# Performance work log

Measured on AMD Instinct MI355X. Metric: run time of the kernel, lower is better.

Reference implementation:

```python
import jax, jax.numpy as jnp
import numpy as np

N, E, H, HEADS, HD, L = 4096, 65536, 128, 4, 32, 4
NF, GF, EF, B = 16, 8, 4, 1


def _ln(x, g, b, eps=1e-5):
    mu = x.mean(-1, keepdims=True)
    v = ((x - mu) ** 2).mean(-1, keepdims=True)
    return (x - mu) * jax.lax.rsqrt(v + eps) * g + b


def _lin(x, W, b=None):
    y = x @ W.T
    return y if b is None else y + b


def _gelu(x):
    return jax.nn.gelu(x, approximate=False)


def setup_inputs() -> dict:
    key = jax.random.key(0)
    ks = iter(jax.random.split(key, 64))
    def rn(shape, s=0.05):
        return jax.random.normal(next(ks), shape, jnp.float32) * s
    inp = {}
    inp['x'] = jax.random.normal(next(ks), (N, NF), jnp.float32)
    inp['edge_index'] = jax.random.randint(next(ks), (2, E), 0, N, dtype=jnp.int32)
    inp['edge_attr'] = jax.random.normal(next(ks), (E, EF), jnp.float32)
    inp['u'] = jax.random.normal(next(ks), (1, GF), jnp.float32)
    inp['acting_mask'] = jax.random.randint(next(ks), (N,), 0, 2, dtype=jnp.int32).astype(bool)
    inp['h_tiles'] = jnp.zeros((N, H), jnp.float32)
    inp['batch'] = jnp.zeros((N,), jnp.int32)
    inp['turn_frac'] = jax.random.uniform(next(ks), (1,), jnp.float32)
    # node / global encoders
    inp['ne_W'] = rn((H, NF + 1)); inp['ne_b'] = jnp.zeros((H,)); inp['ne_g'] = jnp.ones((H,)); inp['ne_be'] = jnp.zeros((H,))
    inp['ge_W'] = rn((H, GF)); inp['ge_b'] = jnp.zeros((H,)); inp['ge_g'] = jnp.ones((H,)); inp['ge_be'] = jnp.zeros((H,))
    # GRUCell
    inp['gru_Wih'] = rn((3 * H, H)); inp['gru_bih'] = jnp.zeros((3 * H,))
    inp['gru_Whh'] = rn((3 * H, H)); inp['gru_bhh'] = jnp.zeros((3 * H,))
    # stacked GATv2 layers
    inp['gat_Wl'] = rn((L, H, H)); inp['gat_bl'] = jnp.zeros((L, H))
    inp['gat_Wr'] = rn((L, H, H)); inp['gat_br'] = jnp.zeros((L, H))
    inp['gat_We'] = rn((L, H, EF))
    inp['gat_att'] = rn((L, HEADS, HD))
    inp['gat_bias'] = jnp.zeros((L, H))
    inp['ln_g'] = jnp.ones((L, H)); inp['ln_b'] = jnp.zeros((L, H))
    # global MHA
    inp['attn_Win'] = rn((3 * H, H)); inp['attn_bin'] = jnp.zeros((3 * H,))
    inp['attn_Wout'] = rn((H, H)); inp['attn_bout'] = jnp.zeros((H,))
    inp['lng_g'] = jnp.ones((H,)); inp['lng_b'] = jnp.zeros((H,))
    # heads (edge_in = 2H + EF)
    inp['mv_W1'] = rn((H, 2 * H + EF)); inp['mv_b1'] = jnp.zeros((H,))
    inp['mv_W2'] = rn((1, H)); inp['mv_b2'] = jnp.zeros((1,))
    inp['fr_W1'] = rn((H, 2 * H + EF)); inp['fr_b1'] = jnp.zeros((H,))
    inp['fr_W2'] = rn((2, H)); inp['fr_b2'] = jnp.zeros((2,))
    inp['vl_W1'] = rn((H, 2 * H)); inp['vl_b1'] = jnp.zeros((H,))
    inp['vl_W2'] = rn((1, H)); inp['vl_b2'] = jnp.zeros((1,))
    return inp


def reference(x, edge_index, edge_attr, u, acting_mask, h_tiles, batch, turn_frac,
              ne_W, ne_b, ne_g, ne_be, ge_W, ge_b, ge_g, ge_be,
              gru_Wih, gru_bih, gru_Whh, gru_bhh,
              gat_Wl, gat_bl, gat_Wr, gat_br, gat_We, gat_att, gat_bias, ln_g, ln_b,
              attn_Win, attn_bin, attn_Wout, attn_bout, lng_g, lng_b,
              mv_W1, mv_b1, mv_W2, mv_b2, fr_W1, fr_b1, fr_W2, fr_b2,
              vl_W1, vl_b1, vl_W2, vl_b2):
    Nn = x.shape[0]
    src, dst = edge_index[0], edge_index[1]
    xa = jnp.concatenate([x, jnp.broadcast_to(turn_frac, (Nn, 1))], -1)
    h = _gelu(_ln(_lin(xa, ne_W, ne_b), ne_g, ne_be))
    ue = _gelu(_ln(_lin(u, ge_W, ge_b), ge_g, ge_be))
    h = h + ue[batch]
    # GRUCell (torch semantics)
    gi = _lin(h, gru_Wih, gru_bih)
    gh = _lin(h_tiles, gru_Whh, gru_bhh)
    i_r, i_z, i_n = jnp.split(gi, 3, -1)
    h_r, h_z, h_n = jnp.split(gh, 3, -1)
    r = jax.nn.sigmoid(i_r + h_r)
    z = jax.nn.sigmoid(i_z + h_z)
    n = jnp.tanh(i_n + r * h_n)
    h = (1.0 - z) * n + z * h_tiles
    h_tiles_new = jax.lax.stop_gradient(h)
    # stacked GATv2 message passing (eval mode: no dropout)
    for l in range(L):
        xl = _lin(h, gat_Wl[l], gat_bl[l]).reshape(Nn, HEADS, HD)   # source messages
        xr = _lin(h, gat_Wr[l], gat_br[l]).reshape(Nn, HEADS, HD)   # target
        ee = (edge_attr @ gat_We[l].T).reshape(-1, HEADS, HD)
        m = xl[src]                                                 # [E,heads,hd]
        s = jax.nn.leaky_relu(m + xr[dst] + ee, negative_slope=0.2)
        score = (s * gat_att[l]).sum(-1)                            # [E,heads]
        mx = jax.ops.segment_max(score, dst, num_segments=Nn)
        mx = jnp.where(jnp.isfinite(mx), mx, 0.0)
        ex = jnp.exp(score - mx[dst])
        den = jax.ops.segment_sum(ex, dst, num_segments=Nn)
        alpha_e = ex / (den[dst] + 1e-16)
        agg = jax.ops.segment_sum(alpha_e[..., None] * m, dst, num_segments=Nn)
        h_mp = agg.reshape(Nn, H) + gat_bias[l]
        h = _ln(h + h_mp, ln_g[l], ln_b[l])
    # global self-attention over all nodes as one sequence
    q, k, v = jnp.split(_lin(h, attn_Win, attn_bin), 3, -1)
    q = q.reshape(Nn, HEADS, HD); k = k.reshape(Nn, HEADS, HD); v = v.reshape(Nn, HEADS, HD)
    att = jax.nn.softmax(jnp.einsum('nhd,mhd->hnm', q, k) / np.float32(np.sqrt(HD)), axis=-1)
    ao = jnp.einsum('hnm,mhd->nhd', att, v).reshape(Nn, H)
    h = _ln(h + _lin(ao, attn_Wout, attn_bout), lng_g, lng_b)
    # edge heads
    eemb = jnp.concatenate([h[src], h[dst], edge_attr], -1)         # [E, 2H+EF]
    move_logits = _lin(_gelu(_lin(eemb, mv_W1, mv_b1)), mv_W2, mv_b2)[:, 0]
    fp = _lin(_gelu(_lin(eemb, fr_W1, fr_b1)), fr_W2, fr_b2)
    alpha = jax.nn.softplus(fp[:, 0]) + 1e-4
    beta = jax.nn.softplus(fp[:, 1]) + 1e-4
    # value head (global mean pool + masked acting pool)
    cnt = jax.ops.segment_sum(jnp.ones((Nn, 1), h.dtype), batch, num_segments=B)
    gpool = jax.ops.segment_sum(h, batch, num_segments=B) / cnt
    ah = jnp.where(acting_mask[:, None], h, 0.0)
    asum = jax.ops.segment_sum(ah, batch, num_segments=B) / cnt
    acnt = jnp.maximum(jax.ops.segment_sum(acting_mask[:, None].astype(h.dtype), batch, num_segments=B) / cnt, 1e-6)
    apool = asum / acnt
    vin = jnp.concatenate([gpool, apool], -1)
    value = _lin(_gelu(_lin(vin, vl_W1, vl_b1)), vl_W2, vl_b2)[:, 0]
    return move_logits, alpha, beta, value, h_tiles_new
```

## Files before the change

### kernel.cpp

```cpp
#include <hip/hip_runtime.h>
#include <math.h>


#define NN 4096
#define EE 65536
#define HH 128
#define NHEADS 4
#define HDIM 32
#define NLAYERS 4
#define NFEAT 16
#define GFEAT 8
#define EFEAT 4
#define KS 4
#define KPAD 296
#define XSTR 136
#define KSTR 40
#define VSTR 72

typedef short bf16x8 __attribute__((ext_vector_type(8)));
typedef float f32x4  __attribute__((ext_vector_type(4)));
union UB { uint4 u; bf16x8 v; };

__device__ __forceinline__ float gelu_f(float x){
  return 0.5f * x * (1.0f + erff(x * 0.7071067811865475f));
}
__device__ __forceinline__ float gelu_fast(float x){
  float u = x + 0.044715f * x * x * x;
  float t = __expf(-1.5957691216f * u);
  return x / (1.0f + t);
}
__device__ __forceinline__ float sigm_fast(float x){ return 1.0f / (1.0f + __expf(-x)); }
__device__ __forceinline__ float tanh_fast(float x){
  float t = __expf(-2.0f * fmaxf(x, -40.0f));
  return 1.0f - 2.0f * t / (1.0f + t);
}
__device__ __forceinline__ float softplus_f(float x){ return x > 20.0f ? x : log1pf(expf(x)); }
__device__ __forceinline__ unsigned short f2bf(float x){
  unsigned u = __float_as_uint(x);
  unsigned r = (u + 0x7FFFu + ((u >> 16) & 1u)) >> 16;
  return (unsigned short)r;
}
__device__ __forceinline__ float bf2f(unsigned short x){
  return __uint_as_float(((unsigned)x) << 16);
}
__device__ __forceinline__ unsigned pack2bf(float lo, float hi){
  unsigned a = (__float_as_uint(lo) + 0x8000u) >> 16;
  unsigned b = (__float_as_uint(hi) + 0x8000u) & 0xFFFF0000u;
  return a | b;
}

__device__ __forceinline__ float block_sum128(float v, float* red){
  int j = threadIdx.x;
  red[j] = v; __syncthreads();
  for (int s = 64; s > 0; s >>= 1){
    if (j < s) red[j] += red[j + s];
    __syncthreads();
  }
  float r = red[0];
  __syncthreads();
  return r;
}

__global__ void k_hist(const int* __restrict__ ei, int* __restrict__ cnt){
  int e = blockIdx.x * 256 + threadIdx.x;
  if (e < EE) atomicAdd(&cnt[ei[EE + e]], 1);
}

__global__ void k_scan(const int* __restrict__ cnt, int* __restrict__ off, int* __restrict__ cur){
  __shared__ int part[256];
  int t = threadIdx.x;
  int local[16];
  int s = 0;
  #pragma unroll
  for (int i = 0; i < 16; i++){ local[i] = s; s += cnt[t * 16 + i]; }
  part[t] = s; __syncthreads();
  for (int o = 1; o < 256; o <<= 1){
    int v = (t >= o) ? part[t - o] : 0;
    __syncthreads();
    part[t] += v;
    __syncthreads();
  }
  int base = part[t] - s;
  #pragma unroll
  for (int i = 0; i < 16; i++){ int o = base + local[i]; off[t * 16 + i] = o; cur[t * 16 + i] = o; }
  if (t == 255) off[NN] = part[255];
}

__global__ void k_scatter(const int* __restrict__ ei, int* __restrict__ cur,
                          int* __restrict__ srcs, int* __restrict__ rank){
  int e = blockIdx.x * 256 + threadIdx.x;
  if (e < EE){
    int d = ei[EE + e];
    int p = atomicAdd(&cur[d], 1);
    srcs[p] = ei[e];
    rank[e] = p;
  }
}

__global__ void k_wprep(const float* __restrict__ Wih, const float* __restrict__ Whh,
                        const float* __restrict__ Wl, const float* __restrict__ Wr,
                        const float* __restrict__ Win, const float* __restrict__ Wout,
                        const float* __restrict__ tiles,
                        const float* __restrict__ bl, const float* __restrict__ br,
                        const float* __restrict__ ea,
                        const float* __restrict__ mvW1, const float* __restrict__ frW1,
                        unsigned short* __restrict__ wbuf, unsigned short* __restrict__ tilesb,
                        float* __restrict__ blrc,
                        unsigned short* __restrict__ wbE, unsigned short* __restrict__ eab,
                        int* __restrict__ cnt, float* __restrict__ gsum){
  int i = blockIdx.x * 256 + threadIdx.x;
  if (i < 49152){ wbuf[i] = f2bf(Wih[i]); }
  else if (i < 98304){ int j = i - 49152; wbuf[49152 + j] = f2bf(Whh[j]); }
  else if (i < 229376){
    int j = i - 98304;
    int l = j >> 15, rem = j & 32767, m = rem >> 7, k = rem & 127;
    float v = (m < 128) ? Wl[l * 16384 + m * 128 + k] : Wr[l * 16384 + (m - 128) * 128 + k];
    wbuf[98304 + j] = f2bf(v);
  }
  else if (i < 278528){ int j = i - 229376; wbuf[229376 + j] = f2bf(Win[j]); }
  else if (i < 294912){ int j = i - 278528; wbuf[278528 + j] = f2bf(Wout[j]); }
  else if (i < 819200){ int j = i - 294912; tilesb[j] = f2bf(tiles[j]); }
  else if (i < 820224){
    int j = i - 819200;
    int l = j >> 8, m = j & 255;
    blrc[j] = (m < 128) ? bl[l * 128 + m] : br[l * 128 + m - 128];
  }
  else if (i < 896000){
    int j = i - 820224;
    int n = j / KPAD, k = j - n * KPAD;
    float v = 0.0f;
    if (k < 2 * HH + EFEAT) v = (n < HH) ? mvW1[n * (2 * HH + EFEAT) + k]
                                         : frW1[(n - HH) * (2 * HH + EFEAT) + k];
    wbE[j] = f2bf(v);
  }
  else if (i < 1158144){
    int j = i - 896000;
    eab[j] = f2bf(ea[j]);
  }
  else if (i < 1162240){ cnt[i - 1158144] = 0; }
  else if (i < 1162497){ gsum[i - 1162240] = 0.0f; }
}

__device__ __forceinline__ void gemm_core(const unsigned short* __restrict__ Xb, int n0,
                                          const unsigned short* __restrict__ Wb, int m0,
                                          unsigned short* Xs, f32x4 acc[8]){
  int t = threadIdx.x;
  #pragma unroll
  for (int k2 = 0; k2 < 4; k2++){
    int v = t + k2 * 256;
    int r = v >> 4, c8 = v & 15;
    *(uint4*)(Xs + r * XSTR + c8 * 8) = *(const uint4*)(Xb + (n0 + r) * 128 + c8 * 8);
  }
  __syncthreads();
  int ln = t & 63, w = t >> 6, lm = ln & 15, quad = ln >> 4;
  const unsigned short* abase = Xs + (16 * w + lm) * XSTR + quad * 8;
  const unsigned short* bbase = Wb + (m0 + lm) * 128 + quad * 8;
  UB af[4];
  #pragma unroll
  for (int ks = 0; ks < 4; ks++) af[ks].u = *(const uint4*)(abase + ks * 32);
  #pragma unroll
  for (int i = 0; i < 8; i++) acc[i] = (f32x4){0.f, 0.f, 0.f, 0.f};
  #pragma unroll
  for (int t2 = 0; t2 < 8; t2++){
    #pragma unroll
    for (int ks = 0; ks < 4; ks++){
      UB bu;
      bu.u = *(const uint4*)(bbase + t2 * 16 * 128 + ks * 32);
      acc[t2] = __builtin_amdgcn_mfma_f32_16x16x32_bf16(af[ks].v, bu.v, acc[t2], 0, 0, 0);
    }
  }
}

__global__ __launch_bounds__(256) void k_gru_lin(const unsigned short* __restrict__ hb,
                                                 const unsigned short* __restrict__ tilesb,
                                                 const unsigned short* __restrict__ Wihb,
                                                 const unsigned short* __restrict__ Whhb,
                                                 const float* __restrict__ bih,
                                                 const float* __restrict__ bhh,
                                                 float* __restrict__ gi, float* __restrict__ gh){
  __shared__ __align__(16) unsigned short Xs[64 * XSTR];
  int z = blockIdx.z;
  const unsigned short* Xb = z ? tilesb : hb;
  const unsigned short* Wb = z ? Whhb : Wihb;
  const float* bias = z ? bhh : bih;
  float* Y = z ? gh : gi;
  int t = threadIdx.x;
  int n0 = blockIdx.x * 64, m0 = blockIdx.y * 128;
  f32x4 acc[8];
  gemm_core(Xb, n0, Wb, m0, Xs, acc);
  int ln = t & 63, w = t >> 6, lm = ln & 15, quad = ln >> 4;
  #pragma unroll
  for (int t2 = 0; t2 < 8; t2++){
    float bv = bias[m0 + t2 * 16 + lm];
    #pragma unroll
    for (int r = 0; r < 4; r++){
      Y[(n0 + 16 * w + quad * 4 + r) * 384 + m0 + t2 * 16 + lm] = acc[t2][r] + bv;
    }
  }
}

__global__ __launch_bounds__(256) void k_lin_gat(const unsigned short* __restrict__ Xb,
                                                 const unsigned short* __restrict__ Wb,
                                                 const float* __restrict__ bias,
                                                 unsigned short* __restrict__ Y,
                                                 float* __restrict__ den){
  __shared__ __align__(16) unsigned short Xs[64 * XSTR];
  int t = threadIdx.x;
  int gid = (blockIdx.y * gridDim.x + blockIdx.x) * 256 + t;
  if (gid < NN * NHEADS) den[gid] = 0.0f;
  int n0 = blockIdx.x * 64, m0 = blockIdx.y * 128;
  f32x4 acc[8];
  gemm_core(Xb, n0, Wb, m0, Xs, acc);
  int ln = t & 63, w = t >> 6, lm = ln & 15, quad = ln >> 4;
  #pragma unroll
  for (int t2 = 0; t2 < 8; t2++){
    float bv = bias[m0 + t2 * 16 + lm];
    #pragma unroll
    for (int r = 0; r < 4; r++){
      Y[(n0 + 16 * w + quad * 4 + r) * 256 + m0 + t2 * 16 + lm] = f2bf(acc[t2][r] + bv);
    }
  }
}

__global__ __launch_bounds__(256) void k_lin_qkv(const unsigned short* __restrict__ Xb,
                                                 const unsigned short* __restrict__ Wb,
                                                 const float* __restrict__ bias,
                                                 unsigned short* __restrict__ qb,
                                                 unsigned short* __restrict__ kb,
                                                 unsigned short* __restrict__ vt){
  __shared__ __align__(16) unsigned short Xs[64 * XSTR];
  int t = threadIdx.x;
  int n0 = blockIdx.x * 64, m0 = blockIdx.y * 128;
  f32x4 acc[8];
  gemm_core(Xb, n0, Wb, m0, Xs, acc);
  int ln = t & 63, w = t >> 6, lm = ln & 15, quad = ln >> 4;
  int nb = n0 + 16 * w + quad * 4;
  const float scale = 0.17677669529663687f;
  if (blockIdx.y == 0){
    #pragma unroll
    for (int t2 = 0; t2 < 8; t2++){
      int m = t2 * 16 + lm;
      float bv = bias[m];
      #pragma unroll
      for (int r = 0; r < 4; r++) qb[(nb + r) * HH + m] = f2bf(acc[t2][r] + bv);
    }
  } else if (blockIdx.y == 1){
    #pragma unroll
    for (int t2 = 0; t2 < 8; t2++){
      int m = t2 * 16 + lm;
      float bv = bias[128 + m];
      #pragma unroll
      for (int r = 0; r < 4; r++) kb[(nb + r) * HH + m] = f2bf((acc[t2][r] + bv) * scale);
    }
  } else {
    #pragma unroll
    for (int t2 = 0; t2 < 8; t2++){
      int m = t2 * 16 + lm;
      float bv = bias[256 + m];
      uint2 p;
      p.x = pack2bf(acc[t2][0] + bv, acc[t2][1] + bv);
      p.y = pack2bf(acc[t2][2] + bv, acc[t2][3] + bv);
      *(uint2*)(vt + m * NN + nb) = p;
    }
  }
}

__global__ void k_node_enc(const float* __restrict__ x, const float* __restrict__ tf,
                           const float* __restrict__ W, const float* __restrict__ b,
                           const float* __restrict__ g, const float* __restrict__ be,
                           const float* __restrict__ u, const float* __restrict__ geW,
                           const float* __restrict__ geb, const float* __restrict__ geg,
                           const float* __restrict__ gebe,
                           float* __restrict__ h, unsigned short* __restrict__ hb){
  __shared__ float red[128];
  __shared__ float xs[NFEAT + 1];
  __shared__ float us[GFEAT];
  int n = blockIdx.x, j = threadIdx.x;
  if (j < NFEAT) xs[j] = x[n * NFEAT + j];
  if (j == NFEAT) xs[NFEAT] = tf[0];
  if (j >= 32 && j < 32 + GFEAT) us[j - 32] = u[j - 32];
  __syncthreads();
  float ua = geb[j];
  #pragma unroll
  for (int k = 0; k < GFEAT; k++) ua += us[k] * geW[j * GFEAT + k];
  float umu = block_sum128(ua, red) * (1.0f / HH);
  float ud = ua - umu;
  float uvar = block_sum128(ud * ud, red) * (1.0f / HH);
  float uej = gelu_f(ud * rsqrtf(uvar + 1e-5f) * geg[j] + gebe[j]);
  float acc = b[j];
  #pragma unroll
  for (int k = 0; k < NFEAT + 1; k++) acc += xs[k] * W[j * (NFEAT + 1) + k];
  float mu = block_sum128(acc, red) * (1.0f / HH);
  float d = acc - mu;
  float var = block_sum128(d * d, red) * (1.0f / HH);
  float r = gelu_f(d * rsqrtf(var + 1e-5f) * g[j] + be[j]) + uej;
  h[n * HH + j] = r;
  hb[n * HH + j] = f2bf(r);
}

__global__ void k_gru_comb(const float* __restrict__ gi, const float* __restrict__ gh,
                           const float* __restrict__ tiles, float* __restrict__ h,
                           unsigned short* __restrict__ hb, float* __restrict__ out_tiles){
  int idx = blockIdx.x * 256 + threadIdx.x;
  int n = idx >> 7, j = idx & 127;
  float ir = gi[n * 384 + j], iz = gi[n * 384 + 128 + j], inn = gi[n * 384 + 256 + j];
  float hr = gh[n * 384 + j], hz = gh[n * 384 + 128 + j], hn = gh[n * 384 + 256 + j];
  float r = sigm_fast(ir + hr), z = sigm_fast(iz + hz);
  float nn2 = tanh_fast(inn + r * hn);
  float ts = tiles[idx];
  float hnew = (1.0f - z) * nn2 + z * ts;
  h[idx] = hnew;
  hb[idx] = f2bf(hnew);
  out_tiles[idx] = hnew;
}

__global__ __launch_bounds__(256) void k_score(const int* __restrict__ ei, const float* __restrict__ ea,
                        const unsigned short* __restrict__ xlrb,
                        const float* __restrict__ We, const float* __restrict__ att,
                        const int* __restrict__ rank,
                        float* __restrict__ exs, float* __restrict__ den){
  __shared__ float4 We4[128];
  __shared__ float atts[128];
  int t = threadIdx.x;
  if (t < 128){ We4[t] = ((const float4*)We)[t]; atts[t] = att[t]; }
  __syncthreads();
  int el = t >> 4, g = t & 15;
  int e = blockIdx.x * 16 + el;
  int s = ei[e], d = ei[EE + e];
  float4 a = *(const float4*)(ea + e * 4);
  UB xlu, xru;
  xlu.u = *(const uint4*)(xlrb + s * 256 + g * 8);
  xru.u = *(const uint4*)(xlrb + d * 256 + 128 + g * 8);
  float sc = 0.0f;
  #pragma unroll
  for (int i = 0; i < 8; i++){
    int j = g * 8 + i;
    float4 w = We4[j];
    float v = bf2f((unsigned short)xlu.v[i]) + bf2f((unsigned short)xru.v[i])
            + a.x * w.x + a.y * w.y + a.z * w.z + a.w * w.w;
    v = v > 0.0f ? v : 0.2f * v;
    sc += v * atts[j];
  }
  sc += __shfl_xor(sc, 1);
  sc += __shfl_xor(sc, 2);
  if ((g & 3) == 0){
    float ev = __expf(sc);
    exs[rank[e] * 4 + (g >> 2)] = ev;
    atomicAdd(&den[d * 4 + (g >> 2)], ev);
  }
}

__global__ __launch_bounds__(256) void k_aggln(
    const unsigned short* __restrict__ xlrb, const float* __restrict__ exs,
    const float* __restrict__ den,
    const int* __restrict__ off, const int* __restrict__ srcs,
    const float* __restrict__ bias, const float* __restrict__ g,
    const float* __restrict__ b, float* __restrict__ h,
    unsigned short* __restrict__ hb){
  int t = threadIdx.x, w = t >> 6, j = t & 63;
  int n = blockIdx.x * 4 + w;
  int p0 = off[n], p1 = off[n + 1];
  int c0 = 2 * j;
  int hh = c0 >> 5;
  float dinv = 1.0f / (den[n * 4 + hh] + 1e-16f);
  float a0 = 0.f, a1 = 0.f;
  int p = p0;
  for (; p + 2 <= p1; p += 2){
    int s0 = srcs[p], s1 = srcs[p + 1];
    float w0 = exs[p * 4 + hh], w1 = exs[(p + 1) * 4 + hh];
    unsigned x0 = *(const unsigned*)(xlrb + s0 * 256 + c0);
    unsigned x1 = *(const unsigned*)(xlrb + s1 * 256 + c0);
    a0 += w0 * bf2f((unsigned short)x0) + w1 * bf2f((unsigned short)x1);
    a1 += w0 * bf2f((unsigned short)(x0 >> 16)) + w1 * bf2f((unsigned short)(x1 >> 16));
  }
  if (p < p1){
    float w0 = exs[p * 4 + hh];
    unsigned x0 = *(const unsigned*)(xlrb + srcs[p] * 256 + c0);
    a0 += w0 * bf2f((unsigned short)x0);
    a1 += w0 * bf2f((unsigned short)(x0 >> 16));
  }
  float2 hv = *(const float2*)(h + n * HH + c0);
  float v0 = hv.x + a0 * dinv + bias[c0];
  float v1 = hv.y + a1 * dinv + bias[c0 + 1];
  float s = v0 + v1;
  #pragma unroll
  for (int d = 1; d < 64; d <<= 1) s += __shfl_xor(s, d);
  float mu = s * (1.0f / HH);
  float d0 = v0 - mu, d1 = v1 - mu;
  float q = d0 * d0 + d1 * d1;
  #pragma unroll
  for (int d = 1; d < 64; d <<= 1) q += __shfl_xor(q, d);
  float rstd = rsqrtf(q * (1.0f / HH) + 1e-5f);
  float o0 = d0 * rstd * g[c0] + b[c0];
  float o1 = d1 * rstd * g[c0 + 1] + b[c0 + 1];
  float2 ov; ov.x = o0; ov.y = o1;
  *(float2*)(h + n * HH + c0) = ov;
  unsigned pk = ((unsigned)f2bf(o0)) | (((unsigned)f2bf(o1)) << 16);
  *(unsigned*)(hb + n * HH + c0) = pk;
}

__global__ __launch_bounds__(256, 4) void k_attn_flash(
    const unsigned short* __restrict__ qb, const unsigned short* __restrict__ kb,
    const unsigned short* __restrict__ vt,
    float* __restrict__ pden, float* __restrict__ pacc){
  __shared__ __align__(16) unsigned short Kls[2][64 * KSTR];
  __shared__ __align__(16) unsigned short Vls[2][32 * VSTR];
  int t = threadIdx.x, w = t >> 6, ln = t & 63;
  int c = ln & 15, qd = ln >> 4;
  int hh = blockIdx.y, ks = blockIdx.z;
  int q0 = blockIdx.x * 64 + w * 16;
  UB qf; qf.u = *(const uint4*)(qb + (q0 + c) * HH + hh * HDIM + qd * 8);
  f32x4 o0a = {0,0,0,0}, o1a = {0,0,0,0}, o0b = {0,0,0,0}, o1b = {0,0,0,0};
  float denp = 0.f;
  int srcA = c + ((qd & 1) << 5);
  int srcB = srcA + 16;
  bool hi = qd >= 2;
  int kk = t >> 2, kp = t & 3;
  int vr = t >> 3, vc = t & 7;
  const unsigned short* kg = kb + hh * HDIM + kp * 8;
  const unsigned short* vg = vt + (hh * HDIM + vr) * NN + vc * 8;

  auto comp = [&](int buf, int hs, f32x4& O0, f32x4& O1){
    UB kf0, kf1, vf0, vf1, pt;
    kf0.u = *(const uint4*)(&Kls[buf][(hs * 32 + c) * KSTR + qd * 8]);
    kf1.u = *(const uint4*)(&Kls[buf][(hs * 32 + 16 + c) * KSTR + qd * 8]);
    vf0.u = *(const uint4*)(&Vls[buf][c * VSTR + hs * 32 + qd * 8]);
    vf1.u = *(const uint4*)(&Vls[buf][(16 + c) * VSTR + hs * 32 + qd * 8]);
    f32x4 s0 = {0,0,0,0}, s1 = {0,0,0,0};
    s0 = __builtin_amdgcn_mfma_f32_16x16x32_bf16(kf0.v, qf.v, s0, 0, 0, 0);
    s1 = __builtin_amdgcn_mfma_f32_16x16x32_bf16(kf1.v, qf.v, s1, 0, 0, 0);
    float e00 = __expf(s0[0]), e01 = __expf(s0[1]), e02 = __expf(s0[2]), e03 = __expf(s0[3]);
    float e10 = __expf(s1[0]), e11 = __expf(s1[1]), e12 = __expf(s1[2]), e13 = __expf(s1[3]);
    denp += (e00 + e01) + (e02 + e03) + (e10 + e11) + (e12 + e13);
    int p00 = (int)pack2bf(e00, e01), p01 = (int)pack2bf(e02, e03);
    int p10 = (int)pack2bf(e10, e11), p11 = (int)pack2bf(e12, e13);
    int a00 = __shfl(p00, srcA), a01 = __shfl(p01, srcA);
    int b00 = __shfl(p00, srcB), b01 = __shfl(p01, srcB);
    int a10 = __shfl(p10, srcA), a11 = __shfl(p11, srcA);
    int b10 = __shfl(p10, srcB), b11 = __shfl(p11, srcB);
    pt.u.x = (unsigned)(hi ? a10 : a00);
    pt.u.y = (unsigned)(hi ? a11 : a01);
    pt.u.z = (unsigned)(hi ? b10 : b00);
    pt.u.w = (unsigned)(hi ? b11 : b01);
    O0 = __builtin_amdgcn_mfma_f32_16x16x32_bf16(vf0.v, pt.v, O0, 0, 0, 0);
    O1 = __builtin_amdgcn_mfma_f32_16x16x32_bf16(vf1.v, pt.v, O1, 0, 0, 0);
  };

  const int kbeg = ks * (NN / KS);
  const int NIT = (NN / KS) / 64;
  {
    uint4 kr = *(const uint4*)(kg + (kbeg + kk) * HH);
    uint4 vr4 = *(const uint4*)(vg + kbeg);
    *(uint4*)(&Kls[0][kk * KSTR + kp * 8]) = kr;
    *(uint4*)(&Vls[0][vr * VSTR + vc * 8]) = vr4;
  }
  __syncthreads();
  for (int it = 0; it < NIT; it++){
    int buf = it & 1;
    if (it + 1 < NIT){
      int kn = kbeg + (it + 1) * 64;
      uint4 kr = *(const uint4*)(kg + (kn + kk) * HH);
      uint4 vr4 = *(const uint4*)(vg + kn);
      comp(buf, 0, o0a, o1a);
      comp(buf, 1, o0b, o1b);
      *(uint4*)(&Kls[buf ^ 1][kk * KSTR + kp * 8]) = kr;
      *(uint4*)(&Vls[buf ^ 1][vr * VSTR + vc * 8]) = vr4;
    } else {
      comp(buf, 0, o0a, o1a);
      comp(buf, 1, o0b, o1b);
    }
    __syncthreads();
  }

  f32x4 o0 = o0a + o0b, o1 = o1a + o1b;
  denp += __shfl_xor(denp, 16);
  denp += __shfl_xor(denp, 32);
  int pi = ((q0 + c) * NHEADS + hh) * KS + ks;
  if (qd == 0) pden[pi] = denp;
  #pragma unroll
  for (int r = 0; r < 4; r++){
    pacc[pi * HDIM + qd * 4 + r]      = o0[r];
    pacc[pi * HDIM + 16 + qd * 4 + r] = o1[r];
  }
}

__global__ __launch_bounds__(256) void k_attn_out(
    const float* __restrict__ pden, const float* __restrict__ pacc,
    const unsigned short* __restrict__ Wb, const float* __restrict__ bout,
    const float* __restrict__ g, const float* __restrict__ b,
    const unsigned char* __restrict__ mask,
    float* __restrict__ h, unsigned short* __restrict__ hb,
    float* __restrict__ gsum, float* __restrict__ msum, float* __restrict__ mcnt){
  __shared__ __align__(16) unsigned short Xs[64 * XSTR];
  __shared__ float colg[128], colm[128], colc;
  int t = threadIdx.x;
  int n0 = blockIdx.x * 64;
  if (t < 128){ colg[t] = 0.f; colm[t] = 0.f; }
  if (t == 128) colc = 0.f;
  for (int idx = t; idx < 64 * 128; idx += 256){
    int r = idx >> 7, j = idx & 127;
    int n = n0 + r, hh = j >> 5, d = j & 31;
    float ds = 0.f, as = 0.f;
    #pragma unroll
    for (int ks2 = 0; ks2 < KS; ks2++){
      int pi = (n * NHEADS + hh) * KS + ks2;
      ds += pden[pi];
      as += pacc[pi * HDIM + d];
    }
    Xs[r * XSTR + j] = f2bf(as / ds);
  }
  __syncthreads();
  int ln = t & 63, w = t >> 6, lm = ln & 15, quad = ln >> 4;
  const unsigned short* abase = Xs + (16 * w + lm) * XSTR + quad * 8;
  const unsigned short* bbase = Wb + lm * 128 + quad * 8;
  UB af[4];
  #pragma unroll
  for (int ks2 = 0; ks2 < 4; ks2++) af[ks2].u = *(const uint4*)(abase + ks2 * 32);
  f32x4 acc[8];
  #pragma unroll
  for (int i = 0; i < 8; i++) acc[i] = (f32x4){0.f, 0.f, 0.f, 0.f};
  #pragma unroll
  for (int t2 = 0; t2 < 8; t2++){
    #pragma unroll
    for (int ks2 = 0; ks2 < 4; ks2++){
      UB bu;
      bu.u = *(const uint4*)(bbase + t2 * 16 * 128 + ks2 * 32);
      acc[t2] = __builtin_amdgcn_mfma_f32_16x16x32_bf16(af[ks2].v, bu.v, acc[t2], 0, 0, 0);
    }
  }
  int nb = n0 + 16 * w + quad * 4;
  float val[8][4];
  #pragma unroll
  for (int t2 = 0; t2 < 8; t2++){
    int m = t2 * 16 + lm;
    float bv = bout[m];
    #pragma unroll
    for (int r = 0; r < 4; r++)
      val[t2][r] = acc[t2][r] + bv + h[(nb + r) * HH + m];
  }
  float mu[4], rs[4];
  #pragma unroll
  for (int r = 0; r < 4; r++){
    float s = 0.f;
    #pragma unroll
    for (int t2 = 0; t2 < 8; t2++) s += val[t2][r];
    s += __shfl_xor(s, 1); s += __shfl_xor(s, 2);
    s += __shfl_xor(s, 4); s += __shfl_xor(s, 8);
    mu[r] = s * (1.0f / HH);
  }
  #pragma unroll
  for (int r = 0; r < 4; r++){
    float s = 0.f;
    #pragma unroll
    for (int t2 = 0; t2 < 8; t2++){ float d2 = val[t2][r] - mu[r]; s += d2 * d2; }
    s += __shfl_xor(s, 1); s += __shfl_xor(s, 2);
    s += __shfl_xor(s, 4); s += __shfl_xor(s, 8);
    rs[r] = rsqrtf(s * (1.0f / HH) + 1e-5f);
  }
  uchar4 mk = *(const uchar4*)(mask + nb);
  float mkf[4] = { mk.x ? 1.f : 0.f, mk.y ? 1.f : 0.f, mk.z ? 1.f : 0.f, mk.w ? 1.f : 0.f };
  #pragma unroll
  for (int t2 = 0; t2 < 8; t2++){
    int m = t2 * 16 + lm;
    float gm = g[m], bm = b[m];
    float sg = 0.f, sm = 0.f;
    #pragma unroll
    for (int r = 0; r < 4; r++){
      float o = (val[t2][r] - mu[r]) * rs[r] * gm + bm;
      h[(nb + r) * HH + m] = o;
      hb[(nb + r) * HH + m] = f2bf(o);
      sg += o;
      sm += mkf[r] * o;
    }
    sg += __shfl_xor(sg, 16); sg += __shfl_xor(sg, 32);
    sm += __shfl_xor(sm, 16); sm += __shfl_xor(sm, 32);
    if (quad == 0){
      atomicAdd(&colg[m], sg);
      atomicAdd(&colm[m], sm);
    }
  }
  if (lm == 0){
    float c = mkf[0] + mkf[1] + mkf[2] + mkf[3];
    atomicAdd(&colc, c);
  }
  __syncthreads();
  if (t < 128){
    atomicAdd(&gsum[t], colg[t]);
    atomicAdd(&msum[t], colm[t]);
  }
  if (t == 128) atomicAdd(mcnt, colc);
}

__global__ __launch_bounds__(256, 4) void k_edge_mfma(
    const unsigned short* __restrict__ hb, const unsigned short* __restrict__ eab,
    const int* __restrict__ ei, const unsigned short* __restrict__ wb,
    const float* __restrict__ mvb1, const float* __restrict__ frb1,
    const float* __restrict__ mvW2, const float* __restrict__ mvb2,
    const float* __restrict__ frW2, const float* __restrict__ frb2,
    float* __restrict__ out){
  __shared__ __align__(16) unsigned short As[64 * KPAD];
  __shared__ float am[64], a0[64], a1[64];
  int t = threadIdx.x;
  int e0 = blockIdx.x * 64;
  if (t < 64){ am[t] = 0.f; a0[t] = 0.f; a1[t] = 0.f; }
  {
    int el = t >> 2, p = t & 3;
    int e = e0 + el;
    int node = (p < 2) ? ei[e] : ei[EE + e];
    int half = p & 1;
    const uint4* srcp = (const uint4*)(hb + node * HH + half * 64);
    uint4* dstp = (uint4*)(As + el * KPAD + (p >> 1) * 128 + half * 64);
    #pragma unroll
    for (int i = 0; i < 8; i++) dstp[i] = srcp[i];
    if (p == 0){
      unsigned short* tail = As + el * KPAD + 256;
      tail[0] = eab[e * 4];     tail[1] = eab[e * 4 + 1];
      tail[2] = eab[e * 4 + 2]; tail[3] = eab[e * 4 + 3];
      #pragma unroll
      for (int i = 4; i < KPAD - 256; i++) tail[i] = 0;
    }
  }
  int ln = t & 63, w = t >> 6, lm = ln & 15, quad = ln >> 4;
  const unsigned short* bbase = wb + (w * 64 + lm) * KPAD + quad * 8;
  f32x4 acc[4][4];
  #pragma unroll
  for (int rt = 0; rt < 4; rt++)
    #pragma unroll
    for (int t2 = 0; t2 < 4; t2++) acc[rt][t2] = (f32x4){0.f, 0.f, 0.f, 0.f};
  __syncthreads();
  #pragma unroll
  for (int ks = 0; ks < 9; ks++){
    UB bf[4], af[4];
    #pragma unroll
    for (int t2 = 0; t2 < 4; t2++) bf[t2].u = *(const uint4*)(bbase + t2 * 16 * KPAD + ks * 32);
    #pragma unroll
    for (int rt = 0; rt < 4; rt++) af[rt].u = *(const uint4*)(As + (16 * rt + lm) * KPAD + quad * 8 + ks * 32);
    #pragma unroll
    for (int rt = 0; rt < 4; rt++)
      #pragma unroll
      for (int t2 = 0; t2 < 4; t2++)
        acc[rt][t2] = __builtin_amdgcn_mfma_f32_16x16x32_bf16(af[rt].v, bf[t2].v, acc[rt][t2], 0, 0, 0);
  }
  if (w < 2){
    #pragma unroll
    for (int rt = 0; rt < 4; rt++){
      #pragma unroll
      for (int r = 0; r < 4; r++){
        float s = 0.f;
        #pragma unroll
        for (int t2 = 0; t2 < 4; t2++){
          int n = w * 64 + t2 * 16 + lm;
          s += gelu_fast(acc[rt][t2][r] + mvb1[n]) * mvW2[n];
        }
        #pragma unroll
        for (int d = 1; d < 16; d <<= 1) s += __shfl_xor(s, d);
        if (lm == 0) atomicAdd(&am[16 * rt + 4 * quad + r], s);
      }
    }
  } else {
    #pragma unroll
    for (int rt = 0; rt < 4; rt++){
      #pragma unroll
      for (int r = 0; r < 4; r++){
        float s0 = 0.f, s1 = 0.f;
        #pragma unroll
        for (int t2 = 0; t2 < 4; t2++){
          int n = (w - 2) * 64 + t2 * 16 + lm;
          float g = gelu_fast(acc[rt][t2][r] + frb1[n]);
          s0 += g * frW2[n];
          s1 += g * frW2[128 + n];
        }
        #pragma unroll
        for (int d = 1; d < 16; d <<= 1){ s0 += __shfl_xor(s0, d); s1 += __shfl_xor(s1, d); }
        if (lm == 0){
          atomicAdd(&a0[16 * rt + 4 * quad + r], s0);
          atomicAdd(&a1[16 * rt + 4 * quad + r], s1);
        }
      }
    }
  }
  __syncthreads();
  if (t < 64){
    int e = e0 + t;
    out[e]          = am[t] + mvb2[0];
    out[EE + e]     = softplus_f(a0[t] + frb2[0]) + 1e-4f;
    out[2 * EE + e] = softplus_f(a1[t] + frb2[1]) + 1e-4f;
  }
}

__global__ void k_value(const float* __restrict__ gsum, const float* __restrict__ msum,
                        const float* __restrict__ mcnt,
                        const float* __restrict__ W1, const float* __restrict__ b1,
                        const float* __restrict__ W2, const float* __restrict__ b2,
                        float* __restrict__ out_val){
  __shared__ float red[128];
  __shared__ float vin[256];
  int j = threadIdx.x;
  float gp = gsum[j] * (1.0f / NN);
  float as = msum[j] * (1.0f / NN);
  float ac = fmaxf(mcnt[0] * (1.0f / NN), 1e-6f);
  vin[j] = gp; vin[HH + j] = as / ac;
  __syncthreads();
  float acc = b1[j];
  const float* w = &W1[j * 256];
  #pragma unroll 4
  for (int k = 0; k < 256; k++) acc += vin[k] * w[k];
  float hv = gelu_f(acc) * W2[j];
  float s = block_sum128(hv, red);
  if (j == 0) out_val[0] = s + b2[0];
}

extern "C" void kernel_launch(void* const* d_in, const int* in_sizes, int n_in,
                              void* d_out, int out_size, void* d_ws, size_t ws_size,
                              hipStream_t stream){
  (void)in_sizes; (void)n_in; (void)out_size; (void)ws_size;
  const float* x        = (const float*)d_in[0];
  const int*   ei       = (const int*)d_in[1];
  const float* ea       = (const float*)d_in[2];
  const float* u        = (const float*)d_in[3];
  const unsigned char* mask = (const unsigned char*)d_in[4];
  const float* tiles    = (const float*)d_in[5];
  const float* tf       = (const float*)d_in[7];
  const float* ne_W  = (const float*)d_in[8];
  const float* ne_b  = (const float*)d_in[9];
  const float* ne_g  = (const float*)d_in[10];
  const float* ne_be = (const float*)d_in[11];
  const float* ge_W  = (const float*)d_in[12];
  const float* ge_b  = (const float*)d_in[13];
  const float* ge_g  = (const float*)d_in[14];
  const float* ge_be = (const float*)d_in[15];
  const float* gru_Wih = (const float*)d_in[16];
  const float* gru_bih = (const float*)d_in[17];
  const float* gru_Whh = (const float*)d_in[18];
  const float* gru_bhh = (const float*)d_in[19];
  const float* gat_Wl  = (const float*)d_in[20];
  const float* gat_bl  = (const float*)d_in[21];
  const float* gat_Wr  = (const float*)d_in[22];
  const float* gat_br  = (const float*)d_in[23];
  const float* gat_We  = (const float*)d_in[24];
  const float* gat_att = (const float*)d_in[25];
  const float* gat_bias= (const float*)d_in[26];
  const float* ln_g    = (const float*)d_in[27];
  const float* ln_b    = (const float*)d_in[28];
  const float* attn_Win = (const float*)d_in[29];
  const float* attn_bin = (const float*)d_in[30];
  const float* attn_Wout= (const float*)d_in[31];
  const float* attn_bout= (const float*)d_in[32];
  const float* lng_g    = (const float*)d_in[33];
  const float* lng_b    = (const float*)d_in[34];
  const float* mv_W1 = (const float*)d_in[35];
  const float* mv_b1 = (const float*)d_in[36];
  const float* mv_W2 = (const float*)d_in[37];
  const float* mv_b2 = (const float*)d_in[38];
  const float* fr_W1 = (const float*)d_in[39];
  const float* fr_b1 = (const float*)d_in[40];
  const float* fr_W2 = (const float*)d_in[41];
  const float* fr_b2 = (const float*)d_in[42];
  const float* vl_W1 = (const float*)d_in[43];
  const float* vl_b1 = (const float*)d_in[44];
  const float* vl_W2 = (const float*)d_in[45];
  const float* vl_b2 = (const float*)d_in[46];

  float* ws = (float*)d_ws;
  float* h      = ws;
  float* xlr    = ws + 524288;
  unsigned short* hb     = (unsigned short*)(ws + 1572864);
  unsigned short* tilesb = (unsigned short*)(ws + 1835008);
  unsigned short* wbuf   = (unsigned short*)(ws + 2097152);
  unsigned short* Wihb  = wbuf;
  unsigned short* Whhb  = wbuf + 49152;
  unsigned short* Wlrb  = wbuf + 98304;
  unsigned short* Winb  = wbuf + 229376;
  unsigned short* Woutb = wbuf + 278528;
  float* blrc   = ws + 2244608;
  float* gsum   = ws + 2245760;
  float* msum   = ws + 2245888;
  float* mcnt   = ws + 2246016;
  int*   cnt    = (int*)(ws + 2246032);
  int*   off    = cnt + NN;
  int*   cur    = off + NN + 1;
  unsigned short* eab = (unsigned short*)(ws + 2323904);
  unsigned short* wbE = (unsigned short*)(ws + 2454976);
  float* S      = ws + 2492864;
  float* gi = S;
  float* gh = S + 1572864;
  float* exs = S;
  int*   srcs = (int*)(S + 262144);
  int*   rank = (int*)(S + 327680);
  unsigned short* xlrb = (unsigned short*)xlr;
  float* den = xlr + 524288;
  unsigned short* qb = (unsigned short*)xlr;
  unsigned short* kb = (unsigned short*)(xlr + 262144);
  unsigned short* vt = (unsigned short*)(xlr + 524288 + 16384);
  float* pacc = S;
  float* pden = S + 2097152;

  float* out       = (float*)d_out;
  float* out_val   = out + 3 * EE;
  float* out_tiles = out + 3 * EE + 1;

  k_wprep<<<(1162497 + 255) / 256, 256, 0, stream>>>(gru_Wih, gru_Whh, gat_Wl, gat_Wr,
                                                     attn_Win, attn_Wout, tiles,
                                                     gat_bl, gat_br, ea, mv_W1, fr_W1,
                                                     wbuf, tilesb, blrc, wbE, eab,
                                                     cnt, gsum);

  k_node_enc<<<NN, 128, 0, stream>>>(x, tf, ne_W, ne_b, ne_g, ne_be,
                                     u, ge_W, ge_b, ge_g, ge_be, h, hb);

  { dim3 g(NN / 64, 3, 2);
    k_gru_lin<<<g, 256, 0, stream>>>(hb, tilesb, Wihb, Whhb, gru_bih, gru_bhh, gi, gh); }
  k_gru_comb<<<NN * HH / 256, 256, 0, stream>>>(gi, gh, tiles, h, hb, out_tiles);

  k_hist   <<<EE / 256, 256, 0, stream>>>(ei, cnt);
  k_scan   <<<1, 256, 0, stream>>>(cnt, off, cur);
  k_scatter<<<EE / 256, 256, 0, stream>>>(ei, cur, srcs, rank);

  for (int l = 0; l < NLAYERS; l++){
    { dim3 g(NN / 64, 2);
      k_lin_gat<<<g, 256, 0, stream>>>(hb, Wlrb + l * 32768, blrc + l * 256, xlrb, den); }
    k_score<<<EE / 16, 256, 0, stream>>>(ei, ea, xlrb,
                                         gat_We + l * HH * EFEAT,
                                         gat_att + l * NHEADS * HDIM, rank, exs, den);
    k_aggln<<<NN / 4, 256, 0, stream>>>(xlrb, exs, den, off, srcs,
                                        gat_bias + l * HH, ln_g + l * HH, ln_b + l * HH, h, hb);
  }

  { dim3 g(NN / 64, 3);
    k_lin_qkv<<<g, 256, 0, stream>>>(hb, Winb, attn_bin, qb, kb, vt); }
  { dim3 gattn(NN / 64, NHEADS, KS);
    k_attn_flash<<<gattn, 256, 0, stream>>>(qb, kb, vt, pden, pacc); }
  k_attn_out<<<NN / 64, 256, 0, stream>>>(pden, pacc, Woutb, attn_bout, lng_g, lng_b,
                                          mask, h, hb, gsum, msum, mcnt);

  k_edge_mfma<<<EE / 64, 256, 0, stream>>>(hb, eab, ei, wbE, mv_b1, fr_b1,
                                           mv_W2, mv_b2, fr_W2, fr_b2, out);

  k_value<<<1, 128, 0, stream>>>(gsum, msum, mcnt, vl_W1, vl_b1, vl_W2, vl_b2, out_val);
}
```

Measured before the change: 399.0 us.

## Fuse GAT edge scoring into CSR aggregation, dropping atomics and score buffer

Removes the separate per-edge score kernel, which did atomic denominator accumulation. Attention logits, exponentials and the softmax denominator are now computed inside the per-destination CSR aggregation kernel. Edge attributes are permuted into CSR order during scatter so the fused loop reads them contiguously, and the rank array, exs buffer and den zeroing go away. In exchange, each edge's score is recomputed with 16-lane shuffle reductions inside the serial per-node loop, which lengthens that loop's critical path.

```diff
diff --git a/kernel.cpp b/kernel.cpp
--- a/kernel.cpp
+++ b/kernel.cpp
@@ -86,14 +86,16 @@
   if (t == 255) off[NN] = part[255];
 }
 
-__global__ void k_scatter(const int* __restrict__ ei, int* __restrict__ cur,
-                          int* __restrict__ srcs, int* __restrict__ rank){
+__global__ void k_scatter(const int* __restrict__ ei, const float* __restrict__ ea,
+                          int* __restrict__ cur,
+                          int* __restrict__ srcs, float* __restrict__ eas4){
   int e = blockIdx.x * 256 + threadIdx.x;
   if (e < EE){
     int d = ei[EE + e];
     int p = atomicAdd(&cur[d], 1);
     srcs[p] = ei[e];
-    rank[e] = p;
+    float4 a = *(const float4*)(ea + e * 4);
+    *(float4*)(eas4 + p * 4) = a;
   }
 }
 
@@ -202,12 +204,9 @@
 __global__ __launch_bounds__(256) void k_lin_gat(const unsigned short* __restrict__ Xb,
                                                  const unsigned short* __restrict__ Wb,
                                                  const float* __restrict__ bias,
-                                                 unsigned short* __restrict__ Y,
-                                                 float* __restrict__ den){
+                                                 unsigned short* __restrict__ Y){
   __shared__ __align__(16) unsigned short Xs[64 * XSTR];
   int t = threadIdx.x;
-  int gid = (blockIdx.y * gridDim.x + blockIdx.x) * 256 + t;
-  if (gid < NN * NHEADS) den[gid] = 0.0f;
   int n0 = blockIdx.x * 64, m0 = blockIdx.y * 128;
   f32x4 acc[8];
   gemm_core(Xb, n0, Wb, m0, Xs, acc);
@@ -314,46 +313,11 @@
   out_tiles[idx] = hnew;
 }
 
-__global__ __launch_bounds__(256) void k_score(const int* __restrict__ ei, const float* __restrict__ ea,
-                        const unsigned short* __restrict__ xlrb,
-                        const float* __restrict__ We, const float* __restrict__ att,
-                        const int* __restrict__ rank,
-                        float* __restrict__ exs, float* __restrict__ den){
-  __shared__ float4 We4[128];
-  __shared__ float atts[128];
-  int t = threadIdx.x;
-  if (t < 128){ We4[t] = ((const float4*)We)[t]; atts[t] = att[t]; }
-  __syncthreads();
-  int el = t >> 4, g = t & 15;
-  int e = blockIdx.x * 16 + el;
-  int s = ei[e], d = ei[EE + e];
-  float4 a = *(const float4*)(ea + e * 4);
-  UB xlu, xru;
-  xlu.u = *(const uint4*)(xlrb + s * 256 + g * 8);
-  xru.u = *(const uint4*)(xlrb + d * 256 + 128 + g * 8);
-  float sc = 0.0f;
-  #pragma unroll
-  for (int i = 0; i < 8; i++){
-    int j = g * 8 + i;
-    float4 w = We4[j];
-    float v = bf2f((unsigned short)xlu.v[i]) + bf2f((unsigned short)xru.v[i])
-            + a.x * w.x + a.y * w.y + a.z * w.z + a.w * w.w;
-    v = v > 0.0f ? v : 0.2f * v;
-    sc += v * atts[j];
-  }
-  sc += __shfl_xor(sc, 1);
-  sc += __shfl_xor(sc, 2);
-  if ((g & 3) == 0){
-    float ev = __expf(sc);
-    exs[rank[e] * 4 + (g >> 2)] = ev;
-    atomicAdd(&den[d * 4 + (g >> 2)], ev);
-  }
-}
-
-__global__ __launch_bounds__(256) void k_aggln(
-    const unsigned short* __restrict__ xlrb, const float* __restrict__ exs,
-    const float* __restrict__ den,
+__global__ __launch_bounds__(256) void k_gat_agg(
+    const unsigned short* __restrict__ xlrb,
     const int* __restrict__ off, const int* __restrict__ srcs,
+    const float* __restrict__ eas4,
+    const float* __restrict__ We, const float* __restrict__ att,
     const float* __restrict__ bias, const float* __restrict__ g,
     const float* __restrict__ b, float* __restrict__ h,
     unsigned short* __restrict__ hb){
@@ -361,24 +325,56 @@
   int n = blockIdx.x * 4 + w;
   int p0 = off[n], p1 = off[n + 1];
   int c0 = 2 * j;
-  int hh = c0 >> 5;
-  float dinv = 1.0f / (den[n * 4 + hh] + 1e-16f);
-  float a0 = 0.f, a1 = 0.f;
+  float4 w0 = ((const float4*)We)[c0];
+  float4 w1 = ((const float4*)We)[c0 + 1];
+  float at0 = att[c0], at1 = att[c0 + 1];
+  unsigned xr = *(const unsigned*)(xlrb + n * 256 + 128 + c0);
+  float xr0 = bf2f((unsigned short)xr), xr1 = bf2f((unsigned short)(xr >> 16));
+  float den = 0.f, a0 = 0.f, a1 = 0.f;
   int p = p0;
   for (; p + 2 <= p1; p += 2){
     int s0 = srcs[p], s1 = srcs[p + 1];
-    float w0 = exs[p * 4 + hh], w1 = exs[(p + 1) * 4 + hh];
+    float4 ev0 = *(const float4*)(eas4 + p * 4);
+    float4 ev1 = *(const float4*)(eas4 + (p + 1) * 4);
     unsigned x0 = *(const unsigned*)(xlrb + s0 * 256 + c0);
     unsigned x1 = *(const unsigned*)(xlrb + s1 * 256 + c0);
-    a0 += w0 * bf2f((unsigned short)x0) + w1 * bf2f((unsigned short)x1);
-    a1 += w0 * bf2f((unsigned short)(x0 >> 16)) + w1 * bf2f((unsigned short)(x1 >> 16));
+    float x00 = bf2f((unsigned short)x0), x01 = bf2f((unsigned short)(x0 >> 16));
+    float x10 = bf2f((unsigned short)x1), x11 = bf2f((unsigned short)(x1 >> 16));
+    float e00 = ev0.x * w0.x + ev0.y * w0.y + ev0.z * w0.z + ev0.w * w0.w;
+    float e01 = ev0.x * w1.x + ev0.y * w1.y + ev0.z * w1.z + ev0.w * w1.w;
+    float e10 = ev1.x * w0.x + ev1.y * w0.y + ev1.z * w0.z + ev1.w * w0.w;
+    float e11 = ev1.x * w1.x + ev1.y * w1.y + ev1.z * w1.z + ev1.w * w1.w;
+    float v00 = x00 + xr0 + e00; v00 = v00 > 0.f ? v00 : 0.2f * v00;
+    float v01 = x01 + xr1 + e01; v01 = v01 > 0.f ? v01 : 0.2f * v01;
+    float v10 = x10 + xr0 + e10; v10 = v10 > 0.f ? v10 : 0.2f * v10;
+    float v11 = x11 + xr1 + e11; v11 = v11 > 0.f ? v11 : 0.2f * v11;
+    float sA = v00 * at0 + v01 * at1;
+    float sB = v10 * at0 + v11 * at1;
+    #pragma unroll
+    for (int d = 1; d < 16; d <<= 1){ sA += __shfl_xor(sA, d); sB += __shfl_xor(sB, d); }
+    float eA = __expf(sA), eB = __expf(sB);
+    den += eA + eB;
+    a0 += eA * x00 + eB * x10;
+    a1 += eA * x01 + eB * x11;
   }
   if (p < p1){
-    float w0 = exs[p * 4 + hh];
-    unsigned x0 = *(const unsigned*)(xlrb + srcs[p] * 256 + c0);
-    a0 += w0 * bf2f((unsigned short)x0);
-    a1 += w0 * bf2f((unsigned short)(x0 >> 16));
-  }
+    int s0 = srcs[p];
+    float4 ev0 = *(const float4*)(eas4 + p * 4);
+    unsigned x0 = *(const unsigned*)(xlrb + s0 * 256 + c0);
+    float x00 = bf2f((unsigned short)x0), x01 = bf2f((unsigned short)(x0 >> 16));
+    float e00 = ev0.x * w0.x + ev0.y * w0.y + ev0.z * w0.z + ev0.w * w0.w;
+    float e01 = ev0.x * w1.x + ev0.y * w1.y + ev0.z * w1.z + ev0.w * w1.w;
+    float v00 = x00 + xr0 + e00; v00 = v00 > 0.f ? v00 : 0.2f * v00;
+    float v01 = x01 + xr1 + e01; v01 = v01 > 0.f ? v01 : 0.2f * v01;
+    float sA = v00 * at0 + v01 * at1;
+    #pragma unroll
+    for (int d = 1; d < 16; d <<= 1) sA += __shfl_xor(sA, d);
+    float eA = __expf(sA);
+    den += eA;
+    a0 += eA * x00;
+    a1 += eA * x01;
+  }
+  float dinv = 1.0f / (den + 1e-16f);
   float2 hv = *(const float2*)(h + n * HH + c0);
   float v0 = hv.x + a0 * dinv + bias[c0];
   float v1 = hv.y + a1 * dinv + bias[c0 + 1];
@@ -784,16 +780,14 @@
   float* S      = ws + 2492864;
   float* gi = S;
   float* gh = S + 1572864;
-  float* exs = S;
+  float* eas4 = S;
   int*   srcs = (int*)(S + 262144);
-  int*   rank = (int*)(S + 327680);
   unsigned short* xlrb = (unsigned short*)xlr;
-  float* den = xlr + 524288;
   unsigned short* qb = (unsigned short*)xlr;
   unsigned short* kb = (unsigned short*)(xlr + 262144);
   unsigned short* vt = (unsigned short*)(xlr + 524288 + 16384);
-  float* pacc = S;
-  float* pden = S + 2097152;
+  float* pacc = S + 327680;
+  float* pden = S + 327680 + 2097152;
 
   float* out       = (float*)d_out;
   float* out_val   = out + 3 * EE;
@@ -814,16 +808,16 @@
 
   k_hist   <<<EE / 256, 256, 0, stream>>>(ei, cnt);
   k_scan   <<<1, 256, 0, stream>>>(cnt, off, cur);
-  k_scatter<<<EE / 256, 256, 0, stream>>>(ei, cur, srcs, rank);
+  k_scatter<<<EE / 256, 256, 0, stream>>>(ei, ea, cur, srcs, eas4);
 
   for (int l = 0; l < NLAYERS; l++){
     { dim3 g(NN / 64, 2);
-      k_lin_gat<<<g, 256, 0, stream>>>(hb, Wlrb + l * 32768, blrc + l * 256, xlrb, den); }
-    k_score<<<EE / 16, 256, 0, stream>>>(ei, ea, xlrb,
-                                         gat_We + l * HH * EFEAT,
-                                         gat_att + l * NHEADS * HDIM, rank, exs, den);
-    k_aggln<<<NN / 4, 256, 0, stream>>>(xlrb, exs, den, off, srcs,
-                                        gat_bias + l * HH, ln_g + l * HH, ln_b + l * HH, h, hb);
+      k_lin_gat<<<g, 256, 0, stream>>>(hb, Wlrb + l * 32768, blrc + l * 256, xlrb); }
+    k_gat_agg<<<NN / 4, 256, 0, stream>>>(xlrb, off, srcs, eas4,
+                                          gat_We + l * HH * EFEAT,
+                                          gat_att + l * NHEADS * HDIM,
+                                          gat_bias + l * HH, ln_g + l * HH, ln_b + l * HH,
+                                          h, hb);
   }
 
   { dim3 g(NN / 64, 3);
```

Measured after the change: 370.4 us. 1.08x faster.
